# Kernel tuning notes

Measured on AMD Instinct MI355X. Metric: run time of the kernel, lower is better.

The kernel has to match this reference:

```python
import jax, jax.numpy as jnp
import numpy as np

SEQ, B, D_IN, D_H, D_OUT = 512, 128, 512, 1024, 256

def _xavier(key, shape):
    fan_out, fan_in = shape
    a = jnp.sqrt(6.0 / (fan_in + fan_out))
    return jax.random.uniform(key, shape, jnp.float32, -a, a)

def setup_inputs() -> dict:
    key = jax.random.key(0)
    k1, k2, k3 = jax.random.split(key, 3)
    x = jax.random.normal(k1, (SEQ, B, D_IN), jnp.float32)
    hidden = jnp.zeros((B, D_H), jnp.float32)
    # i2h: Linear(input+hidden -> hidden); h2o: Linear(hidden -> output)
    W_i2h = _xavier(k2, (D_H, D_IN + D_H))
    b_i2h = jnp.zeros((D_H,), jnp.float32)
    W_h2o = _xavier(k3, (D_OUT, D_H))
    b_h2o = jnp.zeros((D_OUT,), jnp.float32)
    return {"x": x, "hidden": hidden, "W_i2h": W_i2h, "b_i2h": b_i2h, "W_h2o": W_h2o, "b_h2o": b_h2o}

def reference(x, hidden, W_i2h, b_i2h, W_h2o, b_h2o):
    # split i2h weight to avoid materializing the per-step concat
    Wx = W_i2h[:, :x.shape[-1]].T   # [D_in, D_h]
    Wh = W_i2h[:, x.shape[-1]:].T   # [D_h, D_h]
    xW = jnp.einsum('sbi,ih->sbh', x, Wx)  # precompute input projections

    def step(h, xw_t):
        h_new = jnp.tanh(xw_t + h @ Wh + b_i2h)
        return h_new, None

    h_final, _ = jax.lax.scan(step, hidden, xW)
    # only the last timestep's output feeds softmax
    logits = h_final @ W_h2o.T + b_h2o
    class_output = jax.nn.softmax(logits, axis=1)
    return (class_output, h_final)
```

## Files before the change

### kernel.cpp

```cpp
#include <hip/hip_runtime.h>
#include <stdint.h>

typedef __attribute__((ext_vector_type(8))) short short8;
typedef __attribute__((ext_vector_type(4))) float f32x4;
typedef __attribute__((ext_vector_type(4))) unsigned int uint32x4;
typedef unsigned int uint32;
typedef unsigned short ushort16;

#define SEQ 512
#define BATCH 128
#define DIN 512
#define DH 1024
#define DOUT 256

#define XW_OFF   0u
#define XW_BYTES 134217728u
#define WH_OFF   (XW_OFF + XW_BYTES)
#define WH_BYTES 2097152u
#define WX_OFF   (WH_OFF + WH_BYTES)
#define WX_BYTES 1048576u
#define HB_OFF   (WX_OFF + WX_BYTES)
#define HB_BYTES 524288u
#define DN_OFF   (HB_OFF + HB_BYTES)
#define DN_BYTES 262144u

__device__ __forceinline__ ushort16 f2bf(float f) {
  uint32 u = __float_as_uint(f);
  u = u + 0x7fffu + ((u >> 16) & 1u);
  return (ushort16)(u >> 16);
}
__device__ __forceinline__ float bf2f(ushort16 h) {
  return __uint_as_float(((uint32)h) << 16);
}
__device__ __forceinline__ uint32 packbf(float lo, float hi) {
  return (uint32)f2bf(lo) | ((uint32)f2bf(hi) << 16);
}
__device__ __forceinline__ float tanh_fast(float x) {
  float e = __expf(2.0f * x);
  return 1.0f - 2.0f / (e + 1.0f);
}

__global__ __launch_bounds__(256) void prep_kernel(
    const float* __restrict__ W_i2h, const float* __restrict__ hidden,
    ushort16* __restrict__ Wx, ushort16* __restrict__ Wh,
    uint32* __restrict__ hbuf, uint32* __restrict__ flags) {
  int idx = blockIdx.x * 256 + threadIdx.x;
  if (idx < DH * (DIN + DH)) {
    int row = idx / (DIN + DH);
    int col = idx - row * (DIN + DH);
    float v = W_i2h[idx];
    if (col < DIN) Wx[row * DIN + col] = f2bf(v);
    else           Wh[row * DH + (col - DIN)] = f2bf(v);
  }
  if (idx < BATCH * (DH / 2)) {
    int b = idx >> 9, dk = idx & 511;
    hbuf[idx] = packbf(hidden[b * DH + dk * 2], hidden[b * DH + dk * 2 + 1]);
  }
  if (idx < 65536) flags[idx] = 0u;
}

__global__ __launch_bounds__(256) void xw_gemm_kernel(
    const float* __restrict__ x, const ushort16* __restrict__ Wx,
    ushort16* __restrict__ xw) {
  __shared__ __attribute__((aligned(16))) ushort16 Al[128 * 72];
  __shared__ __attribute__((aligned(16))) ushort16 Bl[128 * 72];
  const int tid = threadIdx.x;
  const int lane = tid & 63;
  const int wv = tid >> 6;
  const int mh = wv & 1, nh = wv >> 1;
  const int bm = blockIdx.x >> 3;
  const int bn = blockIdx.x & 7;

  f32x4 acc[4][4];
#pragma unroll
  for (int i = 0; i < 4; ++i)
#pragma unroll
    for (int j = 0; j < 4; ++j) acc[i][j] = (f32x4){0.f, 0.f, 0.f, 0.f};

  uint32* Al32 = (uint32*)Al;

  for (int ko = 0; ko < DIN; ko += 64) {
#pragma unroll
    for (int i = 0; i < 8; ++i) {
      int linear = i * 256 + tid;
      int row = linear >> 4, c4 = linear & 15;
      const float4 v = *(const float4*)(x + (size_t)(bm * 128 + row) * DIN + ko + c4 * 4);
      uint2 p;
      p.x = packbf(v.x, v.y);
      p.y = packbf(v.z, v.w);
      *(uint2*)(Al32 + row * 36 + c4 * 2) = p;
    }
#pragma unroll
    for (int i = 0; i < 4; ++i) {
      int linear = i * 256 + tid;
      int row = linear >> 3, c8 = linear & 7;
      short8 v = *(const short8*)(Wx + (size_t)(bn * 128 + row) * DIN + ko + c8 * 8);
      *(short8*)(Bl + row * 72 + c8 * 8) = v;
    }
    __syncthreads();
#pragma unroll
    for (int kk = 0; kk < 64; kk += 32) {
      short8 af[4], bfv[4];
      const int kb = kk + ((lane >> 4) * 8);
#pragma unroll
      for (int mt = 0; mt < 4; ++mt)
        af[mt] = *(const short8*)(Al + (mh * 64 + mt * 16 + (lane & 15)) * 72 + kb);
#pragma unroll
      for (int nt = 0; nt < 4; ++nt)
        bfv[nt] = *(const short8*)(Bl + (nh * 64 + nt * 16 + (lane & 15)) * 72 + kb);
#pragma unroll
      for (int mt = 0; mt < 4; ++mt)
#pragma unroll
        for (int nt = 0; nt < 4; ++nt)
          acc[mt][nt] = __builtin_amdgcn_mfma_f32_16x16x32_bf16(af[mt], bfv[nt], acc[mt][nt], 0, 0, 0);
    }
    __syncthreads();
  }
#pragma unroll
  for (int mt = 0; mt < 4; ++mt)
#pragma unroll
    for (int nt = 0; nt < 4; ++nt)
#pragma unroll
      for (int r = 0; r < 4; ++r) {
        float v = acc[mt][nt][r];
        float o = __shfl_xor(v, 1);
        if (!(lane & 1)) {
          int m = bm * 128 + mh * 64 + mt * 16 + ((lane >> 4) * 4) + r;
          int c = bn * 128 + nh * 64 + nt * 16 + (lane & 15);
          ((uint32*)xw)[(size_t)m * 512 + (c >> 1)] = packbf(v, o);
        }
      }
}

__global__ __launch_bounds__(256, 1) void rnn_kernel(
    const ushort16* __restrict__ xw, const ushort16* __restrict__ Wh,
    const float* __restrict__ b_i2h,
    uint32* hbuf, uint32* flags, float* __restrict__ h_out) {
  const int g = blockIdx.x & 7;
  const int w = blockIdx.x >> 3;
  const int tid = threadIdx.x;
  const int lane = tid & 63;
  const int q = tid >> 6;
  const int bcol = w * 64 + q * 16 + (lane & 15);
  const int rowloc = (lane >> 4) * 4;

  __shared__ __attribute__((aligned(16))) ushort16 h_lds[16 * 1032];

  short8 bfrag[32];
#pragma unroll
  for (int ks = 0; ks < 32; ++ks)
    bfrag[ks] = *(const short8*)(Wh + (size_t)bcol * DH + ks * 32 + ((lane >> 4) * 8));
  const float biasv = b_i2h[bcol];
  uint32* hl32 = (uint32*)h_lds;
  uint32* fgrp = flags + g * 64;
  const int myflag = w * 4 + q;

  const int r0 = tid >> 7;
  const int c16 = (tid & 127) * 16;
  uint32 voff[8];
#pragma unroll
  for (int j = 0; j < 8; ++j) voff[j] = (uint32)((r0 + 2 * j) * 2048 + c16);
  const uint32* hgrp0 = hbuf + (size_t)g * 16 * 512;
  const uint32* hgrp1 = hbuf + 65536 + (size_t)g * 16 * 512;

  for (int t = 1; t <= SEQ; ++t) {
    const int s = t - 1;
    asm volatile("" : "+v"(bfrag[0]), "+v"(bfrag[1]), "+v"(bfrag[2]), "+v"(bfrag[3]),
                      "+v"(bfrag[4]), "+v"(bfrag[5]), "+v"(bfrag[6]), "+v"(bfrag[7]),
                      "+v"(bfrag[8]), "+v"(bfrag[9]), "+v"(bfrag[10]), "+v"(bfrag[11]),
                      "+v"(bfrag[12]), "+v"(bfrag[13]), "+v"(bfrag[14]), "+v"(bfrag[15]));
    asm volatile("" : "+v"(bfrag[16]), "+v"(bfrag[17]), "+v"(bfrag[18]), "+v"(bfrag[19]),
                      "+v"(bfrag[20]), "+v"(bfrag[21]), "+v"(bfrag[22]), "+v"(bfrag[23]),
                      "+v"(bfrag[24]), "+v"(bfrag[25]), "+v"(bfrag[26]), "+v"(bfrag[27]),
                      "+v"(bfrag[28]), "+v"(bfrag[29]), "+v"(bfrag[30]), "+v"(bfrag[31]));

    float xwv[4];
#pragma unroll
    for (int r = 0; r < 4; ++r)
      xwv[r] = bf2f(xw[(size_t)(s * BATCH + g * 16 + rowloc + r) * DH + bcol]);

    if (t > 1) {
      const uint32 need = (uint32)(t - 1);
      for (;;) {
        uint32 v = __hip_atomic_load(fgrp + lane, __ATOMIC_RELAXED, __HIP_MEMORY_SCOPE_AGENT);
        if (__ballot(v >= need) == ~0ull) break;
      }
    }

    {
      const uint32* hsrc = (s & 1) ? hgrp1 : hgrp0;
      uint32x4 rb[8];
      asm volatile(
          "global_load_dwordx4 %0, %8, %16 sc0 sc1\n\t"
          "global_load_dwordx4 %1, %9, %16 sc0 sc1\n\t"
          "global_load_dwordx4 %2, %10, %16 sc0 sc1\n\t"
          "global_load_dwordx4 %3, %11, %16 sc0 sc1\n\t"
          "global_load_dwordx4 %4, %12, %16 sc0 sc1\n\t"
          "global_load_dwordx4 %5, %13, %16 sc0 sc1\n\t"
          "global_load_dwordx4 %6, %14, %16 sc0 sc1\n\t"
          "global_load_dwordx4 %7, %15, %16 sc0 sc1\n\t"
          "s_waitcnt vmcnt(0)"
          : "=&v"(rb[0]), "=&v"(rb[1]), "=&v"(rb[2]), "=&v"(rb[3]),
            "=&v"(rb[4]), "=&v"(rb[5]), "=&v"(rb[6]), "=&v"(rb[7])
          : "v"(voff[0]), "v"(voff[1]), "v"(voff[2]), "v"(voff[3]),
            "v"(voff[4]), "v"(voff[5]), "v"(voff[6]), "v"(voff[7]),
            "s"(hsrc)
          : "memory");
#pragma unroll
      for (int j = 0; j < 8; ++j)
        *(uint32x4*)(hl32 + (size_t)(r0 + 2 * j) * 516 + (tid & 127) * 4) = rb[j];
    }
    __syncthreads();

    f32x4 acc0 = (f32x4){0.f, 0.f, 0.f, 0.f};
    f32x4 acc1 = (f32x4){0.f, 0.f, 0.f, 0.f};
#pragma unroll
    for (int ks = 0; ks < 16; ++ks) {
      short8 af0 = *(const short8*)((const char*)h_lds +
                    (lane & 15) * 2064 + (2 * ks) * 64 + ((lane >> 4) * 16));
      short8 af1 = *(const short8*)((const char*)h_lds +
                    (lane & 15) * 2064 + (2 * ks + 1) * 64 + ((lane >> 4) * 16));
      acc0 = __builtin_amdgcn_mfma_f32_16x16x32_bf16(af0, bfrag[2 * ks], acc0, 0, 0, 0);
      acc1 = __builtin_amdgcn_mfma_f32_16x16x32_bf16(af1, bfrag[2 * ks + 1], acc1, 0, 0, 0);
    }

    float hv[4];
#pragma unroll
    for (int r = 0; r < 4; ++r)
      hv[r] = tanh_fast(acc0[r] + acc1[r] + biasv + xwv[r]);

    {
      uint32* hdst = (uint32*)((t & 1) ? hgrp1 : hgrp0);
#pragma unroll
      for (int r = 0; r < 4; ++r) {
        float o = __shfl_xor(hv[r], 1);
        uint32 pk = packbf(hv[r], o);
        if (!(lane & 1)) {
          uint32* p = hdst + (size_t)(rowloc + r) * 512 + (bcol >> 1);
          asm volatile("global_store_dword %0, %1, off sc0 sc1"
                       :: "v"(p), "v"(pk) : "memory");
        }
      }
    }
    if (t == SEQ) {
#pragma unroll
      for (int r = 0; r < 4; ++r)
        h_out[(size_t)(g * 16 + rowloc + r) * DH + bcol] = hv[r];
    }
    asm volatile("s_waitcnt vmcnt(0)" ::: "memory");
    if (lane == 0) {
      uint32* fp = fgrp + myflag;
      uint32 tv = (uint32)t;
      asm volatile("global_store_dword %0, %1, off sc0 sc1"
                   :: "v"(fp), "v"(tv) : "memory");
    }
  }
}

__global__ __launch_bounds__(256) void head_kernel(
    const float* __restrict__ hfin, const float* __restrict__ W,
    const float* __restrict__ bias, float* __restrict__ out) {
  __shared__ __attribute__((aligned(16))) float hrow[DH];
  __shared__ float rbuf[256];
  const int b = blockIdx.x;
  const int tid = threadIdx.x;
  for (int i = tid; i < DH; i += 256) hrow[i] = hfin[(size_t)b * DH + i];
  __syncthreads();
  float s = bias[tid];
  const float4* wr = (const float4*)(W + (size_t)tid * DH);
#pragma unroll 4
  for (int k = 0; k < DH / 4; ++k) {
    float4 wv = wr[k];
    float4 hv = *(const float4*)(hrow + k * 4);
    s += wv.x * hv.x + wv.y * hv.y + wv.z * hv.z + wv.w * hv.w;
  }
  rbuf[tid] = s;
  __syncthreads();
  for (int off = 128; off > 0; off >>= 1) {
    if (tid < off) rbuf[tid] = fmaxf(rbuf[tid], rbuf[tid + off]);
    __syncthreads();
  }
  float mx = rbuf[0];
  __syncthreads();
  float e = __expf(s - mx);
  rbuf[tid] = e;
  __syncthreads();
  for (int off = 128; off > 0; off >>= 1) {
    if (tid < off) rbuf[tid] += rbuf[tid + off];
    __syncthreads();
  }
  out[(size_t)b * DOUT + tid] = e / rbuf[0];
}

extern "C" void kernel_launch(void* const* d_in, const int* in_sizes, int n_in,
                              void* d_out, int out_size, void* d_ws, size_t ws_size,
                              hipStream_t stream) {
  const float* x      = (const float*)d_in[0];
  const float* hidden = (const float*)d_in[1];
  const float* W_i2h  = (const float*)d_in[2];
  const float* b_i2h  = (const float*)d_in[3];
  const float* W_h2o  = (const float*)d_in[4];
  const float* b_h2o  = (const float*)d_in[5];
  float* out = (float*)d_out;

  char* ws = (char*)d_ws;
  ushort16* xw    = (ushort16*)(ws + XW_OFF);
  ushort16* Wh    = (ushort16*)(ws + WH_OFF);
  ushort16* Wx    = (ushort16*)(ws + WX_OFF);
  uint32*   hbuf  = (uint32*)(ws + HB_OFF);
  uint32*   flags = (uint32*)(ws + DN_OFF);

  prep_kernel<<<6144, 256, 0, stream>>>(W_i2h, hidden, Wx, Wh, hbuf, flags);
  xw_gemm_kernel<<<4096, 256, 0, stream>>>(x, Wx, xw);
  rnn_kernel<<<128, 256, 0, stream>>>(xw, Wh, b_i2h, hbuf, flags, out + BATCH * DOUT);
  head_kernel<<<128, 256, 0, stream>>>(out + BATCH * DOUT, W_h2o, b_h2o, out);
}
```

Before: 2.164 ms.

## Tag hidden-state words with step counter to validate reads without waiting on stores

```diff
diff --git a/kernel.cpp b/kernel.cpp
--- a/kernel.cpp
+++ b/kernel.cpp
@@ -4,6 +4,7 @@
 typedef __attribute__((ext_vector_type(8))) short short8;
 typedef __attribute__((ext_vector_type(4))) float f32x4;
 typedef __attribute__((ext_vector_type(4))) unsigned int uint32x4;
+typedef __attribute__((ext_vector_type(2))) unsigned int uint32x2;
 typedef unsigned int uint32;
 typedef unsigned short ushort16;
 
@@ -20,7 +21,7 @@
 #define WX_OFF   (WH_OFF + WH_BYTES)
 #define WX_BYTES 1048576u
 #define HB_OFF   (WX_OFF + WX_BYTES)
-#define HB_BYTES 524288u
+#define HB_BYTES 1048576u
 #define DN_OFF   (HB_OFF + HB_BYTES)
 #define DN_BYTES 262144u
 
@@ -43,7 +44,7 @@
 __global__ __launch_bounds__(256) void prep_kernel(
     const float* __restrict__ W_i2h, const float* __restrict__ hidden,
     ushort16* __restrict__ Wx, ushort16* __restrict__ Wh,
-    uint32* __restrict__ hbuf, uint32* __restrict__ flags) {
+    uint32x2* __restrict__ hpair, uint32* __restrict__ flags) {
   int idx = blockIdx.x * 256 + threadIdx.x;
   if (idx < DH * (DIN + DH)) {
     int row = idx / (DIN + DH);
@@ -54,7 +55,7 @@
   }
   if (idx < BATCH * (DH / 2)) {
     int b = idx >> 9, dk = idx & 511;
-    hbuf[idx] = packbf(hidden[b * DH + dk * 2], hidden[b * DH + dk * 2 + 1]);
+    hpair[idx] = (uint32x2){packbf(hidden[b * DH + dk * 2], hidden[b * DH + dk * 2 + 1]), 0u};
   }
   if (idx < 65536) flags[idx] = 0u;
 }
@@ -135,7 +136,7 @@
 __global__ __launch_bounds__(256, 1) void rnn_kernel(
     const ushort16* __restrict__ xw, const ushort16* __restrict__ Wh,
     const float* __restrict__ b_i2h,
-    uint32* hbuf, uint32* flags, float* __restrict__ h_out) {
+    uint32x2* hpair, uint32* flags, float* __restrict__ h_out) {
   const int g = blockIdx.x & 7;
   const int w = blockIdx.x >> 3;
   const int tid = threadIdx.x;
@@ -155,13 +156,11 @@
   uint32* fgrp = flags + g * 64;
   const int myflag = w * 4 + q;
 
-  const int r0 = tid >> 7;
-  const int c16 = (tid & 127) * 16;
-  uint32 voff[8];
-#pragma unroll
-  for (int j = 0; j < 8; ++j) voff[j] = (uint32)((r0 + 2 * j) * 2048 + c16);
-  const uint32* hgrp0 = hbuf + (size_t)g * 16 * 512;
-  const uint32* hgrp1 = hbuf + 65536 + (size_t)g * 16 * 512;
+  uint32 voffp[16];
+#pragma unroll
+  for (int j = 0; j < 16; ++j) voffp[j] = (uint32)((tid + 256 * j) * 16);
+  const uint32x2* pg0 = hpair + (size_t)g * 16 * 512;
+  const uint32x2* pg1 = hpair + 65536 + (size_t)g * 16 * 512;
 
   for (int t = 1; t <= SEQ; ++t) {
     const int s = t - 1;
@@ -188,57 +187,85 @@
     }
 
     {
-      const uint32* hsrc = (s & 1) ? hgrp1 : hgrp0;
-      uint32x4 rb[8];
-      asm volatile(
-          "global_load_dwordx4 %0, %8, %16 sc0 sc1\n\t"
-          "global_load_dwordx4 %1, %9, %16 sc0 sc1\n\t"
-          "global_load_dwordx4 %2, %10, %16 sc0 sc1\n\t"
-          "global_load_dwordx4 %3, %11, %16 sc0 sc1\n\t"
-          "global_load_dwordx4 %4, %12, %16 sc0 sc1\n\t"
-          "global_load_dwordx4 %5, %13, %16 sc0 sc1\n\t"
-          "global_load_dwordx4 %6, %14, %16 sc0 sc1\n\t"
-          "global_load_dwordx4 %7, %15, %16 sc0 sc1\n\t"
-          "s_waitcnt vmcnt(0)"
-          : "=&v"(rb[0]), "=&v"(rb[1]), "=&v"(rb[2]), "=&v"(rb[3]),
-            "=&v"(rb[4]), "=&v"(rb[5]), "=&v"(rb[6]), "=&v"(rb[7])
-          : "v"(voff[0]), "v"(voff[1]), "v"(voff[2]), "v"(voff[3]),
-            "v"(voff[4]), "v"(voff[5]), "v"(voff[6]), "v"(voff[7]),
-            "s"(hsrc)
-          : "memory");
-#pragma unroll
-      for (int j = 0; j < 8; ++j)
-        *(uint32x4*)(hl32 + (size_t)(r0 + 2 * j) * 516 + (tid & 127) * 4) = rb[j];
+      const uint32x2* hsrc = (s & 1) ? pg1 : pg0;
+      const uint32 su = (uint32)s;
+      uint32x4 rb[16];
+      for (;;) {
+        asm volatile(
+            "global_load_dwordx4 %0, %16, %32 sc0 sc1\n\t"
+            "global_load_dwordx4 %1, %17, %32 sc0 sc1\n\t"
+            "global_load_dwordx4 %2, %18, %32 sc0 sc1\n\t"
+            "global_load_dwordx4 %3, %19, %32 sc0 sc1\n\t"
+            "global_load_dwordx4 %4, %20, %32 sc0 sc1\n\t"
+            "global_load_dwordx4 %5, %21, %32 sc0 sc1\n\t"
+            "global_load_dwordx4 %6, %22, %32 sc0 sc1\n\t"
+            "global_load_dwordx4 %7, %23, %32 sc0 sc1\n\t"
+            "global_load_dwordx4 %8, %24, %32 sc0 sc1\n\t"
+            "global_load_dwordx4 %9, %25, %32 sc0 sc1\n\t"
+            "global_load_dwordx4 %10, %26, %32 sc0 sc1\n\t"
+            "global_load_dwordx4 %11, %27, %32 sc0 sc1\n\t"
+            "global_load_dwordx4 %12, %28, %32 sc0 sc1\n\t"
+            "global_load_dwordx4 %13, %29, %32 sc0 sc1\n\t"
+            "global_load_dwordx4 %14, %30, %32 sc0 sc1\n\t"
+            "global_load_dwordx4 %15, %31, %32 sc0 sc1\n\t"
+            "s_waitcnt vmcnt(0)"
+            : "=&v"(rb[0]), "=&v"(rb[1]), "=&v"(rb[2]), "=&v"(rb[3]),
+              "=&v"(rb[4]), "=&v"(rb[5]), "=&v"(rb[6]), "=&v"(rb[7]),
+              "=&v"(rb[8]), "=&v"(rb[9]), "=&v"(rb[10]), "=&v"(rb[11]),
+              "=&v"(rb[12]), "=&v"(rb[13]), "=&v"(rb[14]), "=&v"(rb[15])
+            : "v"(voffp[0]), "v"(voffp[1]), "v"(voffp[2]), "v"(voffp[3]),
+              "v"(voffp[4]), "v"(voffp[5]), "v"(voffp[6]), "v"(voffp[7]),
+              "v"(voffp[8]), "v"(voffp[9]), "v"(voffp[10]), "v"(voffp[11]),
+              "v"(voffp[12]), "v"(voffp[13]), "v"(voffp[14]), "v"(voffp[15]),
+              "s"(hsrc)
+            : "memory");
+        uint32 bad = 0;
+#pragma unroll
+        for (int j = 0; j < 16; ++j)
+          bad |= (rb[j][1] ^ su) | (rb[j][3] ^ su);
+        if (bad == 0) break;
+      }
+#pragma unroll
+      for (int j = 0; j < 16; ++j) {
+        int p = tid + 256 * j;
+        *(uint32x2*)(hl32 + (p >> 8) * 516 + (p & 255) * 2) =
+            (uint32x2){rb[j][0], rb[j][2]};
+      }
     }
     __syncthreads();
 
     f32x4 acc0 = (f32x4){0.f, 0.f, 0.f, 0.f};
     f32x4 acc1 = (f32x4){0.f, 0.f, 0.f, 0.f};
-#pragma unroll
-    for (int ks = 0; ks < 16; ++ks) {
-      short8 af0 = *(const short8*)((const char*)h_lds +
-                    (lane & 15) * 2064 + (2 * ks) * 64 + ((lane >> 4) * 16));
-      short8 af1 = *(const short8*)((const char*)h_lds +
-                    (lane & 15) * 2064 + (2 * ks + 1) * 64 + ((lane >> 4) * 16));
-      acc0 = __builtin_amdgcn_mfma_f32_16x16x32_bf16(af0, bfrag[2 * ks], acc0, 0, 0, 0);
-      acc1 = __builtin_amdgcn_mfma_f32_16x16x32_bf16(af1, bfrag[2 * ks + 1], acc1, 0, 0, 0);
+    f32x4 acc2 = (f32x4){0.f, 0.f, 0.f, 0.f};
+    f32x4 acc3 = (f32x4){0.f, 0.f, 0.f, 0.f};
+#pragma unroll
+    for (int ks = 0; ks < 8; ++ks) {
+      const char* base = (const char*)h_lds + (lane & 15) * 2064 + ((lane >> 4) * 16);
+      short8 af0 = *(const short8*)(base + (4 * ks + 0) * 64);
+      short8 af1 = *(const short8*)(base + (4 * ks + 1) * 64);
+      short8 af2 = *(const short8*)(base + (4 * ks + 2) * 64);
+      short8 af3 = *(const short8*)(base + (4 * ks + 3) * 64);
+      acc0 = __builtin_amdgcn_mfma_f32_16x16x32_bf16(af0, bfrag[4 * ks + 0], acc0, 0, 0, 0);
+      acc1 = __builtin_amdgcn_mfma_f32_16x16x32_bf16(af1, bfrag[4 * ks + 1], acc1, 0, 0, 0);
+      acc2 = __builtin_amdgcn_mfma_f32_16x16x32_bf16(af2, bfrag[4 * ks + 2], acc2, 0, 0, 0);
+      acc3 = __builtin_amdgcn_mfma_f32_16x16x32_bf16(af3, bfrag[4 * ks + 3], acc3, 0, 0, 0);
     }
 
     float hv[4];
 #pragma unroll
     for (int r = 0; r < 4; ++r)
-      hv[r] = tanh_fast(acc0[r] + acc1[r] + biasv + xwv[r]);
+      hv[r] = tanh_fast((acc0[r] + acc1[r]) + (acc2[r] + acc3[r]) + biasv + xwv[r]);
 
     {
-      uint32* hdst = (uint32*)((t & 1) ? hgrp1 : hgrp0);
+      uint32x2* hdst = (uint32x2*)((t & 1) ? pg1 : pg0);
 #pragma unroll
       for (int r = 0; r < 4; ++r) {
         float o = __shfl_xor(hv[r], 1);
-        uint32 pk = packbf(hv[r], o);
+        uint32x2 val = {packbf(hv[r], o), (uint32)t};
         if (!(lane & 1)) {
-          uint32* p = hdst + (size_t)(rowloc + r) * 512 + (bcol >> 1);
-          asm volatile("global_store_dword %0, %1, off sc0 sc1"
-                       :: "v"(p), "v"(pk) : "memory");
+          uint32x2* p = hdst + (size_t)(rowloc + r) * 512 + (bcol >> 1);
+          asm volatile("global_store_dwordx2 %0, %1, off sc0 sc1"
+                       :: "v"(p), "v"(val) : "memory");
         }
       }
     }
@@ -247,7 +274,6 @@
       for (int r = 0; r < 4; ++r)
         h_out[(size_t)(g * 16 + rowloc + r) * DH + bcol] = hv[r];
     }
-    asm volatile("s_waitcnt vmcnt(0)" ::: "memory");
     if (lane == 0) {
       uint32* fp = fgrp + myflag;
       uint32 tv = (uint32)t;
@@ -307,11 +333,11 @@
   ushort16* xw    = (ushort16*)(ws + XW_OFF);
   ushort16* Wh    = (ushort16*)(ws + WH_OFF);
   ushort16* Wx    = (ushort16*)(ws + WX_OFF);
-  uint32*   hbuf  = (uint32*)(ws + HB_OFF);
+  uint32x2* hpair = (uint32x2*)(ws + HB_OFF);
   uint32*   flags = (uint32*)(ws + DN_OFF);
 
-  prep_kernel<<<6144, 256, 0, stream>>>(W_i2h, hidden, Wx, Wh, hbuf, flags);
+  prep_kernel<<<6144, 256, 0, stream>>>(W_i2h, hidden, Wx, Wh, hpair, flags);
   xw_gemm_kernel<<<4096, 256, 0, stream>>>(x, Wx, xw);
-  rnn_kernel<<<128, 256, 0, stream>>>(xw, Wh, b_i2h, hbuf, flags, out + BATCH * DOUT);
+  rnn_kernel<<<128, 256, 0, stream>>>(xw, Wh, b_i2h, hpair, flags, out + BATCH * DOUT);
   head_kernel<<<128, 256, 0, stream>>>(out + BATCH * DOUT, W_h2o, b_h2o, out);
 }
```

After: 2.237 ms. 1.03x slower.
